# Kernel optimization log

Measured on AMD Instinct MI355X. Metric: run time of the kernel, lower is better.

The kernel has to match this reference:

```python
import jax, jax.numpy as jnp
import numpy as np
from jax import lax

CURRICULUM_EP = 12
LI, LS, LW = 0.5, 0.8, 3.0


def _gauss_win(ws, C, dtype):
    coords = jnp.arange(ws, dtype=jnp.float32) - ws // 2
    g = jnp.exp(-coords ** 2 / (2 * 1.5 ** 2))
    win = g[None, :] * g[:, None]
    win = win / win.sum()
    # depthwise kernel, OIHW with I=1, O=C
    return jnp.broadcast_to(win[None, None], (C, 1, ws, ws)).astype(dtype)


def _dwconv(x, win, p, C):
    return lax.conv_general_dilated(
        x, win, window_strides=(1, 1), padding=[(p, p), (p, p)],
        dimension_numbers=('NCHW', 'OIHW', 'NCHW'), feature_group_count=C)


def diff_ssim(x, y, ws=11):
    C1, C2 = 0.01 ** 2, 0.03 ** 2
    C = x.shape[1]
    p = ws // 2
    win = _gauss_win(ws, C, x.dtype)
    mx = _dwconv(x, win, p, C)
    my = _dwconv(y, win, p, C)
    sxx = _dwconv(x * x, win, p, C) - mx ** 2
    syy = _dwconv(y * y, win, p, C) - my ** 2
    sxy = _dwconv(x * y, win, p, C) - mx * my
    ssim_map = (2 * mx * my + C1) * (2 * sxy + C2) / ((mx ** 2 + my ** 2 + C1) * (sxx + syy + C2))
    return ssim_map.mean()


def setup_inputs() -> dict:
    key = jax.random.key(0)
    k1, k2, k3, k4 = jax.random.split(key, 4)
    B, C, H, W = 16, 3, 512, 512
    NB = 1024  # watermark bits
    eps = 1e-4
    cover = jax.random.uniform(k1, (B, C, H, W), dtype=jnp.float32)
    wmed = jax.random.uniform(k2, (B, C, H, W), dtype=jnp.float32)
    wm_orig = jax.random.uniform(k3, (B, NB), dtype=jnp.float32)
    wm_ext = jnp.clip(jax.random.uniform(k4, (B, NB), dtype=jnp.float32), eps, 1.0 - eps)
    return {"cover": cover, "wmed": wmed, "wm_orig": wm_orig, "wm_ext": wm_ext, "epoch": 20}


def reference(cover, wmed, wm_orig, wm_ext, epoch):
    ml = jnp.mean((wmed - cover) ** 2)
    sv = diff_ssim(wmed, cover)
    sl = 1.0 - sv
    wl = jnp.mean(-(wm_orig * jnp.log(wm_ext) + (1.0 - wm_orig) * jnp.log(1.0 - wm_ext)))
    if epoch <= CURRICULUM_EP:
        w_img, w_ssim = 0.05, 0.05
    else:
        progress = min(1.0, (epoch - CURRICULUM_EP) / 10.0)
        w_img = 0.05 + (LI - 0.05) * progress
        w_ssim = 0.05 + (LS - 0.05) * progress
    total = w_img * ml + w_ssim * sl + LW * wl
    return (total, ml, sv, wl)
```

## Files before the change

### kernel.cpp

```cpp
#include <hip/hip_runtime.h>
#include <math.h>

#define H_IMG 512
#define W_IMG 512
#define TH 32
#define TW 32
#define HALO 5
#define WS11 11
#define SH (TH + 2*HALO)
#define NTHREADS 256

#define RWF 33
#define RWR (5*RWF)
#define RBUF_N (SH*RWR)

#define W0 0.00102838f
#define W1 0.00759873f
#define W2 0.03600075f
#define W3 0.10936070f
#define W4 0.21300556f
#define W5 0.26601172f
__device__ __constant__ float c_w[WS11] = {W0,W1,W2,W3,W4,W5,W4,W3,W2,W1,W0};

__global__ __launch_bounds__(NTHREADS) void ssim_mse_tile(
        const float* __restrict__ cover, const float* __restrict__ wmed,
        float* __restrict__ part, int nParts) {
    __shared__ __align__(16) float rbuf[RBUF_N];
    __shared__ float red[8];

    const int tid = threadIdx.x;
    const size_t pbase = (size_t)blockIdx.z * (H_IMG*W_IMG);
    const float* xp = wmed + pbase;
    const float* yp = cover + pbase;
    const int ty0 = blockIdx.y*TH - HALO;
    const int tx0 = blockIdx.x*TW - HALO;
    const bool xin = (blockIdx.x != 0) && (blockIdx.x != gridDim.x - 1);

    float mse_acc = 0.f;
    for (int t = tid; t < SH*8; t += NTHREADS) {
        const int r = t >> 3, c0 = (t & 7) << 2;
        const int gy = ty0 + r;
        const bool rok = (unsigned)gy < (unsigned)H_IMG;
        const int gc = tx0 + c0;
        const float* prx = xp + (size_t)(rok ? gy : 0) * W_IMG + gc;
        const float* pry = yp + (size_t)(rok ? gy : 0) * W_IMG + gc;
        float xv[14], yv[14];
        if (rok && xin) {
#pragma unroll
            for (int j = 0; j < 14; ++j) { xv[j] = prx[j]; yv[j] = pry[j]; }
        } else if (rok) {
#pragma unroll
            for (int j = 0; j < 14; ++j) {
                bool ok = (unsigned)(gc + j) < (unsigned)W_IMG;
                xv[j] = ok ? prx[j] : 0.f;
                yv[j] = ok ? pry[j] : 0.f;
            }
        } else {
#pragma unroll
            for (int j = 0; j < 14; ++j) { xv[j] = 0.f; yv[j] = 0.f; }
        }

        if (rok && r >= HALO && r < HALO+TH) {
#pragma unroll
            for (int j = 5; j < 9; ++j) {
                float d = xv[j] - yv[j];
                mse_acc = fmaf(d, d, mse_acc);
            }
        }

        float a0[4]={0,0,0,0}, a1[4]={0,0,0,0}, a2[4]={0,0,0,0};
        float a3[4]={0,0,0,0}, a4[4]={0,0,0,0};
#pragma unroll
        for (int j = 0; j < 14; ++j) {
            float px = xv[j], py = yv[j];
            float pxx = px*px, pyy = py*py, pxy = px*py;
#pragma unroll
            for (int k = 0; k < 4; ++k) {
                int tap = j - k;
                if (tap >= 0 && tap < WS11) {
                    float wv = c_w[tap];
                    a0[k] = fmaf(wv, px,  a0[k]);
                    a1[k] = fmaf(wv, py,  a1[k]);
                    a2[k] = fmaf(wv, pxx, a2[k]);
                    a3[k] = fmaf(wv, pyy, a3[k]);
                    a4[k] = fmaf(wv, pxy, a4[k]);
                }
            }
        }
        float* wb = &rbuf[r*RWR + c0];
#pragma unroll
        for (int k = 0; k < 4; ++k) {
            wb[0*RWF + k] = a0[k];
            wb[1*RWF + k] = a1[k];
            wb[2*RWF + k] = a2[k];
            wb[3*RWF + k] = a3[k];
            wb[4*RWF + k] = a4[k];
        }
    }
    __syncthreads();

    const float C1 = 0.01f*0.01f, C2 = 0.03f*0.03f;
    const int c  = tid & 31;
    const int r0 = (tid >> 5) << 2;
    float m0[4]={0,0,0,0}, m1[4]={0,0,0,0}, e2[4]={0,0,0,0};
    float e3[4]={0,0,0,0}, e4[4]={0,0,0,0};
#pragma unroll
    for (int i = 0; i < 14; ++i) {
        const float* rb = &rbuf[(r0 + i)*RWR + c];
        float v0 = rb[0*RWF], v1 = rb[1*RWF], v2 = rb[2*RWF];
        float v3 = rb[3*RWF], v4 = rb[4*RWF];
#pragma unroll
        for (int k = 0; k < 4; ++k) {
            int tap = i - k;
            if (tap >= 0 && tap < WS11) {
                float wv = c_w[tap];
                m0[k] = fmaf(wv, v0, m0[k]);
                m1[k] = fmaf(wv, v1, m1[k]);
                e2[k] = fmaf(wv, v2, e2[k]);
                e3[k] = fmaf(wv, v3, e3[k]);
                e4[k] = fmaf(wv, v4, e4[k]);
            }
        }
    }
    float ssim_acc = 0.f;
#pragma unroll
    for (int k = 0; k < 4; ++k) {
        float mx = m0[k], my = m1[k];
        float sxx = e2[k] - mx*mx;
        float syy = e3[k] - my*my;
        float sxy = e4[k] - mx*my;
        float num = (2.f*mx*my + C1) * (2.f*sxy + C2);
        float den = (mx*mx + my*my + C1) * (sxx + syy + C2);
        ssim_acc += __fdividef(num, den);
    }

#pragma unroll
    for (int off = 32; off > 0; off >>= 1) {
        ssim_acc += __shfl_down(ssim_acc, off);
        mse_acc  += __shfl_down(mse_acc, off);
    }
    int wid = tid >> 6, lane = tid & 63;
    if (lane == 0) { red[wid] = ssim_acc; red[4+wid] = mse_acc; }
    __syncthreads();
    if (tid == 0) {
        float s = red[0]+red[1]+red[2]+red[3];
        float m = red[4]+red[5]+red[6]+red[7];
        int bid = (blockIdx.z*gridDim.y + blockIdx.y)*gridDim.x + blockIdx.x;
        part[bid] = s;
        part[nParts + bid] = m;
    }
}

#define FT 1024
__global__ __launch_bounds__(FT) void finalize_k(
        const float* __restrict__ part, int nParts,
        const float* __restrict__ wm_orig, const float* __restrict__ wm_ext,
        int nWm, const int* __restrict__ epoch_p,
        float* __restrict__ out, double inv_npix, double inv_nwm) {
    __shared__ double red[48];
    int tid = threadIdx.x;
    double s_ssim = 0.0, s_mse = 0.0, s_wl = 0.0;
    const float4* s4 = (const float4*)part;
    const float4* m4 = (const float4*)(part + nParts);
    int n4 = nParts >> 2;
    for (int i = tid; i < n4; i += FT) {
        float4 v = s4[i];
        s_ssim += (double)((v.x + v.y) + (v.z + v.w));
        float4 u = m4[i];
        s_mse  += (double)((u.x + u.y) + (u.z + u.w));
    }
    const float4* p4 = (const float4*)wm_orig;
    const float4* q4 = (const float4*)wm_ext;
    int w4 = nWm >> 2;
    for (int i = tid; i < w4; i += FT) {
        float4 p = p4[i], q = q4[i];
        float a;
        a  = -(p.x*__logf(q.x) + (1.f-p.x)*__logf(1.f-q.x));
        a += -(p.y*__logf(q.y) + (1.f-p.y)*__logf(1.f-q.y));
        a += -(p.z*__logf(q.z) + (1.f-p.z)*__logf(1.f-q.z));
        a += -(p.w*__logf(q.w) + (1.f-p.w)*__logf(1.f-q.w));
        s_wl += (double)a;
    }
#pragma unroll
    for (int off = 32; off > 0; off >>= 1) {
        s_ssim += __shfl_down(s_ssim, off);
        s_mse  += __shfl_down(s_mse, off);
        s_wl   += __shfl_down(s_wl, off);
    }
    int wid = tid >> 6, lane = tid & 63;
    if (lane == 0) { red[wid] = s_ssim; red[16+wid] = s_mse; red[32+wid] = s_wl; }
    __syncthreads();
    if (tid == 0) {
        double ssim_sum = 0.0, mse_sum = 0.0, wl_sum = 0.0;
        for (int i = 0; i < 16; ++i) {
            ssim_sum += red[i]; mse_sum += red[16+i]; wl_sum += red[32+i];
        }
        float sv = (float)(ssim_sum * inv_npix);
        float ml = (float)(mse_sum  * inv_npix);
        float wl = (float)(wl_sum   * inv_nwm);
        int e = *epoch_p;
        float w_img, w_ssim;
        if (e <= 12) {
            w_img = 0.05f; w_ssim = 0.05f;
        } else {
            float progress = fminf(1.0f, (float)(e - 12) / 10.0f);
            w_img  = 0.05f + (0.5f - 0.05f)*progress;
            w_ssim = 0.05f + (0.8f - 0.05f)*progress;
        }
        float sl = 1.0f - sv;
        float total = w_img*ml + w_ssim*sl + 3.0f*wl;
        out[0] = total;
        out[1] = ml;
        out[2] = sv;
        out[3] = wl;
    }
}

extern "C" void kernel_launch(void* const* d_in, const int* in_sizes, int n_in,
                              void* d_out, int out_size, void* d_ws, size_t ws_size,
                              hipStream_t stream) {
    const float* cover   = (const float*)d_in[0];
    const float* wmed    = (const float*)d_in[1];
    const float* wm_orig = (const float*)d_in[2];
    const float* wm_ext  = (const float*)d_in[3];
    const int*   epoch   = (const int*)d_in[4];
    float* out = (float*)d_out;

    int npix   = in_sizes[0];
    int planes = npix / (H_IMG * W_IMG);
    int nWm    = in_sizes[2];

    dim3 grid(W_IMG/TW, H_IMG/TH, planes);
    int nParts = grid.x * grid.y * grid.z;
    float* part = (float*)d_ws;

    ssim_mse_tile<<<grid, NTHREADS, 0, stream>>>(cover, wmed, part, nParts);
    finalize_k<<<1, FT, 0, stream>>>(part, nParts, wm_orig, wm_ext, nWm,
                                     epoch, out,
                                     1.0 / (double)npix, 1.0 / (double)nWm);
}
```

Baseline: 206.5 us.

## Process four tiles per block with float4 halo loads and occupancy hint

Each block now loops over four consecutive 32x32 tiles on a 1D grid, so there are a quarter as many blocks and partial sums. Interior rows are loaded with aligned float4 vector loads plus one scalar load instead of fourteen scalar loads. A min-blocks-per-CU launch bound is added. This aims to cut per-block launch and reduction overhead and improve load efficiency, but it serializes tiles within a block, adds an extra barrier per tile, and may constrain register allocation.

After: 198.5 us. -3.9%, faster.

```diff
diff --git a/kernel.cpp b/kernel.cpp
--- a/kernel.cpp
+++ b/kernel.cpp
@@ -9,6 +9,7 @@
 #define WS11 11
 #define SH (TH + 2*HALO)
 #define NTHREADS 256
+#define TPB 4
 
 #define RWF 33
 #define RWR (5*RWF)
@@ -22,116 +23,142 @@
 #define W5 0.26601172f
 __device__ __constant__ float c_w[WS11] = {W0,W1,W2,W3,W4,W5,W4,W3,W2,W1,W0};
 
-__global__ __launch_bounds__(NTHREADS) void ssim_mse_tile(
+__global__ __launch_bounds__(NTHREADS, 5) void ssim_mse_tile(
         const float* __restrict__ cover, const float* __restrict__ wmed,
         float* __restrict__ part, int nParts) {
     __shared__ __align__(16) float rbuf[RBUF_N];
     __shared__ float red[8];
 
     const int tid = threadIdx.x;
-    const size_t pbase = (size_t)blockIdx.z * (H_IMG*W_IMG);
-    const float* xp = wmed + pbase;
-    const float* yp = cover + pbase;
-    const int ty0 = blockIdx.y*TH - HALO;
-    const int tx0 = blockIdx.x*TW - HALO;
-    const bool xin = (blockIdx.x != 0) && (blockIdx.x != gridDim.x - 1);
-
-    float mse_acc = 0.f;
-    for (int t = tid; t < SH*8; t += NTHREADS) {
-        const int r = t >> 3, c0 = (t & 7) << 2;
-        const int gy = ty0 + r;
-        const bool rok = (unsigned)gy < (unsigned)H_IMG;
-        const int gc = tx0 + c0;
-        const float* prx = xp + (size_t)(rok ? gy : 0) * W_IMG + gc;
-        const float* pry = yp + (size_t)(rok ? gy : 0) * W_IMG + gc;
-        float xv[14], yv[14];
-        if (rok && xin) {
-#pragma unroll
-            for (int j = 0; j < 14; ++j) { xv[j] = prx[j]; yv[j] = pry[j]; }
-        } else if (rok) {
+    float ssim_acc = 0.f, mse_acc = 0.f;
+
+    for (int it = 0; it < TPB; ++it) {
+        const int tile = blockIdx.x * TPB + it;
+        const int bx = tile & 15;
+        const int by = (tile >> 4) & 15;
+        const int pl = tile >> 8;
+        const size_t pbase = (size_t)pl * (H_IMG*W_IMG);
+        const float* xp = wmed + pbase;
+        const float* yp = cover + pbase;
+        const int ty0 = by*TH - HALO;
+        const int tx0 = bx*TW - HALO;
+        const bool xin = (bx != 0) && (bx != 15);
+
+        for (int t = tid; t < SH*8; t += NTHREADS) {
+            const int r = t >> 3, c0 = (t & 7) << 2;
+            const int gy = ty0 + r;
+            const bool rok = (unsigned)gy < (unsigned)H_IMG;
+            float xv[14], yv[14];
+            if (rok && xin) {
+                const int ga = tx0 + c0 - 3;
+                const float* rx = xp + (size_t)gy*W_IMG + ga;
+                const float* ry = yp + (size_t)gy*W_IMG + ga;
+                float4 XA = *(const float4*)(rx);
+                float4 XB = *(const float4*)(rx + 4);
+                float4 XC = *(const float4*)(rx + 8);
+                float4 XD = *(const float4*)(rx + 12);
+                float  XE = rx[16];
+                float4 YA = *(const float4*)(ry);
+                float4 YB = *(const float4*)(ry + 4);
+                float4 YC = *(const float4*)(ry + 8);
+                float4 YD = *(const float4*)(ry + 12);
+                float  YE = ry[16];
+                xv[0]=XA.w;  xv[1]=XB.x;  xv[2]=XB.y;  xv[3]=XB.z;  xv[4]=XB.w;
+                xv[5]=XC.x;  xv[6]=XC.y;  xv[7]=XC.z;  xv[8]=XC.w;  xv[9]=XD.x;
+                xv[10]=XD.y; xv[11]=XD.z; xv[12]=XD.w; xv[13]=XE;
+                yv[0]=YA.w;  yv[1]=YB.x;  yv[2]=YB.y;  yv[3]=YB.z;  yv[4]=YB.w;
+                yv[5]=YC.x;  yv[6]=YC.y;  yv[7]=YC.z;  yv[8]=YC.w;  yv[9]=YD.x;
+                yv[10]=YD.y; yv[11]=YD.z; yv[12]=YD.w; yv[13]=YE;
+            } else if (rok) {
+                const int gc = tx0 + c0;
+                const float* prx = xp + (size_t)gy*W_IMG + gc;
+                const float* pry = yp + (size_t)gy*W_IMG + gc;
+#pragma unroll
+                for (int j = 0; j < 14; ++j) {
+                    bool ok = (unsigned)(gc + j) < (unsigned)W_IMG;
+                    xv[j] = ok ? prx[j] : 0.f;
+                    yv[j] = ok ? pry[j] : 0.f;
+                }
+            } else {
+#pragma unroll
+                for (int j = 0; j < 14; ++j) { xv[j] = 0.f; yv[j] = 0.f; }
+            }
+
+            if (rok && r >= HALO && r < HALO+TH) {
+#pragma unroll
+                for (int j = 5; j < 9; ++j) {
+                    float d = xv[j] - yv[j];
+                    mse_acc = fmaf(d, d, mse_acc);
+                }
+            }
+
+            float a0[4]={0,0,0,0}, a1[4]={0,0,0,0}, a2[4]={0,0,0,0};
+            float a3[4]={0,0,0,0}, a4[4]={0,0,0,0};
 #pragma unroll
             for (int j = 0; j < 14; ++j) {
-                bool ok = (unsigned)(gc + j) < (unsigned)W_IMG;
-                xv[j] = ok ? prx[j] : 0.f;
-                yv[j] = ok ? pry[j] : 0.f;
-            }
-        } else {
-#pragma unroll
-            for (int j = 0; j < 14; ++j) { xv[j] = 0.f; yv[j] = 0.f; }
-        }
-
-        if (rok && r >= HALO && r < HALO+TH) {
-#pragma unroll
-            for (int j = 5; j < 9; ++j) {
-                float d = xv[j] - yv[j];
-                mse_acc = fmaf(d, d, mse_acc);
-            }
-        }
-
-        float a0[4]={0,0,0,0}, a1[4]={0,0,0,0}, a2[4]={0,0,0,0};
-        float a3[4]={0,0,0,0}, a4[4]={0,0,0,0};
-#pragma unroll
-        for (int j = 0; j < 14; ++j) {
-            float px = xv[j], py = yv[j];
-            float pxx = px*px, pyy = py*py, pxy = px*py;
+                float px = xv[j], py = yv[j];
+                float pxx = px*px, pyy = py*py, pxy = px*py;
+#pragma unroll
+                for (int k = 0; k < 4; ++k) {
+                    int tap = j - k;
+                    if (tap >= 0 && tap < WS11) {
+                        float wv = c_w[tap];
+                        a0[k] = fmaf(wv, px,  a0[k]);
+                        a1[k] = fmaf(wv, py,  a1[k]);
+                        a2[k] = fmaf(wv, pxx, a2[k]);
+                        a3[k] = fmaf(wv, pyy, a3[k]);
+                        a4[k] = fmaf(wv, pxy, a4[k]);
+                    }
+                }
+            }
+            float* wb = &rbuf[r*RWR + c0];
 #pragma unroll
             for (int k = 0; k < 4; ++k) {
-                int tap = j - k;
-                if (tap >= 0 && tap < WS11) {
-                    float wv = c_w[tap];
-                    a0[k] = fmaf(wv, px,  a0[k]);
-                    a1[k] = fmaf(wv, py,  a1[k]);
-                    a2[k] = fmaf(wv, pxx, a2[k]);
-                    a3[k] = fmaf(wv, pyy, a3[k]);
-                    a4[k] = fmaf(wv, pxy, a4[k]);
-                }
-            }
-        }
-        float* wb = &rbuf[r*RWR + c0];
-#pragma unroll
-        for (int k = 0; k < 4; ++k) {
-            wb[0*RWF + k] = a0[k];
-            wb[1*RWF + k] = a1[k];
-            wb[2*RWF + k] = a2[k];
-            wb[3*RWF + k] = a3[k];
-            wb[4*RWF + k] = a4[k];
-        }
-    }
-    __syncthreads();
-
-    const float C1 = 0.01f*0.01f, C2 = 0.03f*0.03f;
-    const int c  = tid & 31;
-    const int r0 = (tid >> 5) << 2;
-    float m0[4]={0,0,0,0}, m1[4]={0,0,0,0}, e2[4]={0,0,0,0};
-    float e3[4]={0,0,0,0}, e4[4]={0,0,0,0};
-#pragma unroll
-    for (int i = 0; i < 14; ++i) {
-        const float* rb = &rbuf[(r0 + i)*RWR + c];
-        float v0 = rb[0*RWF], v1 = rb[1*RWF], v2 = rb[2*RWF];
-        float v3 = rb[3*RWF], v4 = rb[4*RWF];
-#pragma unroll
-        for (int k = 0; k < 4; ++k) {
-            int tap = i - k;
-            if (tap >= 0 && tap < WS11) {
-                float wv = c_w[tap];
-                m0[k] = fmaf(wv, v0, m0[k]);
-                m1[k] = fmaf(wv, v1, m1[k]);
-                e2[k] = fmaf(wv, v2, e2[k]);
-                e3[k] = fmaf(wv, v3, e3[k]);
-                e4[k] = fmaf(wv, v4, e4[k]);
-            }
-        }
-    }
-    float ssim_acc = 0.f;
-#pragma unroll
-    for (int k = 0; k < 4; ++k) {
-        float mx = m0[k], my = m1[k];
-        float sxx = e2[k] - mx*mx;
-        float syy = e3[k] - my*my;
-        float sxy = e4[k] - mx*my;
-        float num = (2.f*mx*my + C1) * (2.f*sxy + C2);
-        float den = (mx*mx + my*my + C1) * (sxx + syy + C2);
-        ssim_acc += __fdividef(num, den);
+                wb[0*RWF + k] = a0[k];
+                wb[1*RWF + k] = a1[k];
+                wb[2*RWF + k] = a2[k];
+                wb[3*RWF + k] = a3[k];
+                wb[4*RWF + k] = a4[k];
+            }
+        }
+        __syncthreads();
+
+        {
+            const float C1 = 0.01f*0.01f, C2 = 0.03f*0.03f;
+            const int c  = tid & 31;
+            const int r0 = (tid >> 5) << 2;
+            float m0[4]={0,0,0,0}, m1[4]={0,0,0,0}, e2[4]={0,0,0,0};
+            float e3[4]={0,0,0,0}, e4[4]={0,0,0,0};
+#pragma unroll
+            for (int i = 0; i < 14; ++i) {
+                const float* rb = &rbuf[(r0 + i)*RWR + c];
+                float v0 = rb[0*RWF], v1 = rb[1*RWF], v2 = rb[2*RWF];
+                float v3 = rb[3*RWF], v4 = rb[4*RWF];
+#pragma unroll
+                for (int k = 0; k < 4; ++k) {
+                    int tap = i - k;
+                    if (tap >= 0 && tap < WS11) {
+                        float wv = c_w[tap];
+                        m0[k] = fmaf(wv, v0, m0[k]);
+                        m1[k] = fmaf(wv, v1, m1[k]);
+                        e2[k] = fmaf(wv, v2, e2[k]);
+                        e3[k] = fmaf(wv, v3, e3[k]);
+                        e4[k] = fmaf(wv, v4, e4[k]);
+                    }
+                }
+            }
+#pragma unroll
+            for (int k = 0; k < 4; ++k) {
+                float mx = m0[k], my = m1[k];
+                float sxx = e2[k] - mx*mx;
+                float syy = e3[k] - my*my;
+                float sxy = e4[k] - mx*my;
+                float num = (2.f*mx*my + C1) * (2.f*sxy + C2);
+                float den = (mx*mx + my*my + C1) * (sxx + syy + C2);
+                ssim_acc += __fdividef(num, den);
+            }
+        }
+        __syncthreads();
     }
 
 #pragma unroll
@@ -145,9 +172,8 @@
     if (tid == 0) {
         float s = red[0]+red[1]+red[2]+red[3];
         float m = red[4]+red[5]+red[6]+red[7];
-        int bid = (blockIdx.z*gridDim.y + blockIdx.y)*gridDim.x + blockIdx.x;
-        part[bid] = s;
-        part[nParts + bid] = m;
+        part[blockIdx.x] = s;
+        part[nParts + blockIdx.x] = m;
     }
 }
 
@@ -230,11 +256,12 @@
     int planes = npix / (H_IMG * W_IMG);
     int nWm    = in_sizes[2];
 
-    dim3 grid(W_IMG/TW, H_IMG/TH, planes);
-    int nParts = grid.x * grid.y * grid.z;
+    int nTiles  = 16 * 16 * planes;
+    int nBlocks = nTiles / TPB;
+    int nParts  = nBlocks;
     float* part = (float*)d_ws;
 
-    ssim_mse_tile<<<grid, NTHREADS, 0, stream>>>(cover, wmed, part, nParts);
+    ssim_mse_tile<<<nBlocks, NTHREADS, 0, stream>>>(cover, wmed, part, nParts);
     finalize_k<<<1, FT, 0, stream>>>(part, nParts, wm_orig, wm_ext, nWm,
                                      epoch, out,
                                      1.0 / (double)npix, 1.0 / (double)nWm);
```
